# Kernel tuning notes

Measured on AMD Instinct MI355X. Metric: run time of the kernel, lower is better.

The kernel has to match this reference:

```python
import jax, jax.numpy as jnp
import numpy as np

B, T, D, P = 4, 2048, 1024, 128

def setup_inputs() -> dict:
    key = jax.random.key(0)
    ks = jax.random.split(key, 10)
    inp = {
        "x": jax.random.normal(ks[0], (B, T, D), dtype=jnp.float32),
        "Q_filt": jax.random.normal(ks[1], (P, P), dtype=jnp.float32),
        "K_filt": jax.random.normal(ks[2], (P, P), dtype=jnp.float32),
        "W_in": jax.random.normal(ks[3], (D, P), dtype=jnp.float32) / np.sqrt(D),
        "b_in": jax.random.normal(ks[4], (P,), dtype=jnp.float32) * 0.01,
        "W_v": jax.random.normal(ks[5], (D, P), dtype=jnp.float32) / np.sqrt(D),
        "b_v": jax.random.normal(ks[6], (P,), dtype=jnp.float32) * 0.01,
        "W_o": jax.random.normal(ks[7], (P, D), dtype=jnp.float32) / np.sqrt(P),
        "b_o": jax.random.normal(ks[8], (D,), dtype=jnp.float32) * 0.01,
        "decay": jnp.ones((T,), dtype=jnp.float32),
    }
    return inp

def reference(x, Q_filt, K_filt, W_in, b_in, W_v, b_v, W_o, b_o, decay):
    # x: (B,T,D)
    x_proj = x @ W_in + b_in          # (B,T,P)
    Q = x_proj @ Q_filt               # (B,T,P)
    K = x_proj @ K_filt               # (B,T,P)
    V = x @ W_v + b_v                 # (B,T,P)
    # outer-product state per timestep, scaled by per-step decay
    Z = jnp.einsum('bti,btj->btij', V, K) * decay[None, :, None, None]
    H = jnp.cumsum(Z, axis=1)         # (B,T,P,P) cumulative linear-attn state
    Y = jnp.einsum('bti,btij->btj', Q, H)  # (B,T,P)
    return Y @ W_o + b_o              # (B,T,D)
```

## Files before the change

kernel.cpp:

```cpp
#include <hip/hip_runtime.h>

#define BB 4
#define TT 2048
#define DD 1024
#define PP 128
#define NC 16
#define CH 128

typedef __attribute__((ext_vector_type(8))) short bf16x8;
typedef __attribute__((ext_vector_type(4))) float f32x4;

__device__ inline ushort f2bf(float f) {
  unsigned u = __builtin_bit_cast(unsigned, f);
  u = (u + 0x7FFF + ((u >> 16) & 1)) >> 16;
  return (ushort)u;
}

__device__ inline void gll16(const void* g, void* l) {
  __builtin_amdgcn_global_load_lds(
      (const __attribute__((address_space(1))) void*)g,
      (__attribute__((address_space(3))) void*)l, 16, 0, 0);
}

__device__ inline int swzoff(int row, int kbyte) {
  return row * 256 + (kbyte ^ ((row & 7) << 4));
}

template <int NI, int NT>
__device__ inline void stage_swz(const ushort* __restrict__ g, int ld, int koff,
                                 char* lds, int tid) {
#pragma unroll
  for (int j = 0; j < NI; ++j) {
    int L = j * (NT * 16) + tid * 16;
    int row = L >> 8;
    int off = (L & 255) ^ ((row & 7) << 4);
    gll16(g + (size_t)row * ld + koff + (off >> 1),
          lds + j * (NT * 16) + ((tid & (NT - 64)) << 4));
  }
}

__device__ inline bf16x8 ld_swz(const char* lds, int row, int kbyte) {
  return *(const bf16x8*)(lds + swzoff(row, kbyte));
}

__device__ inline bf16x8 pack8(const float4& a, const float4& b) {
  bf16x8 v;
  v[0] = (short)f2bf(a.x); v[1] = (short)f2bf(a.y);
  v[2] = (short)f2bf(a.z); v[3] = (short)f2bf(a.w);
  v[4] = (short)f2bf(b.x); v[5] = (short)f2bf(b.y);
  v[6] = (short)f2bf(b.z); v[7] = (short)f2bf(b.w);
  return v;
}

__global__ __launch_bounds__(256) void prep_w(
    const float* __restrict__ Qf, const float* __restrict__ Kf,
    const float* __restrict__ W_in, const float* __restrict__ b_in,
    const float* __restrict__ W_v, const float* __restrict__ b_v,
    const float* __restrict__ W_o, ushort* __restrict__ WcatT,
    ushort* __restrict__ QKcT, ushort* __restrict__ WoT,
    float* __restrict__ bcat) {
  int i = blockIdx.x * 256 + threadIdx.x;
  if (i < 262144) {
    int n = i & 255, k = i >> 8;
    float v = (n < 128) ? W_in[k * 128 + n] : W_v[k * 128 + (n - 128)];
    WcatT[(size_t)n * 1024 + k] = f2bf(v);
  } else if (i < 294912) {
    int j = i - 262144;
    int n = j & 255, k = j >> 8;
    float v = (n < 128) ? Qf[k * 128 + n] : Kf[k * 128 + (n - 128)];
    QKcT[n * 128 + k] = f2bf(v);
  } else if (i < 425984) {
    int j = i - 294912;
    int n = j & 1023, k = j >> 10;
    WoT[(size_t)n * 128 + k] = f2bf(W_o[(size_t)k * 1024 + n]);
  } else if (i < 426240) {
    int j = i - 425984;
    bcat[j] = (j < 128) ? b_in[j] : b_v[j - 128];
  }
}

__global__ __launch_bounds__(512) void gemm_xw(
    const float* __restrict__ x, const ushort* __restrict__ WcatT,
    const float* __restrict__ bcat, ushort* __restrict__ XP,
    ushort* __restrict__ V, ushort* __restrict__ VT) {
  __shared__ char sm[2][49152];
  const int bid = blockIdx.x;
  const int swz = (bid & 7) * 32 + (bid >> 3);
  const int bm = (swz >> 1) * 64;
  const int bn = (swz & 1) * 128;
  const int tid = threadIdx.x, w = tid >> 6, l = tid & 63;
  const int wr = w >> 2, wc = w & 3, lr = l & 15, lk = l >> 4;

  const int arow = tid >> 3;
  const int acol = (tid & 7) * 16;
  const float* Ax = x + (size_t)(bm + arow) * DD + acol;
  const ushort* Bg = WcatT + (size_t)bn * DD;

  float4 ra[4];
  f32x4 z = {0.f, 0.f, 0.f, 0.f};
  f32x4 acc[2][2];
#pragma unroll
  for (int m = 0; m < 2; ++m)
#pragma unroll
    for (int n = 0; n < 2; ++n) acc[m][n] = z;

#define LOADA(t)                                                  \
  {                                                               \
    const float4* p = (const float4*)(Ax + (((t) & 7) << 7));     \
    _Pragma("unroll") for (int j = 0; j < 4; ++j) ra[j] = p[j];   \
  }
#define WRITEA(lds)                                               \
  {                                                               \
    *(bf16x8*)((lds) + swzoff(arow, acol * 2)) = pack8(ra[0], ra[1]); \
    *(bf16x8*)((lds) + swzoff(arow, acol * 2 + 16)) = pack8(ra[2], ra[3]); \
  }

  LOADA(0);
  stage_swz<4, 512>(Bg, DD, 0, sm[0] + 16384, tid);
  asm volatile("s_waitcnt vmcnt(4)" ::: "memory");
  WRITEA(sm[0]);
  LOADA(1);

  int cur = 0;
  for (int t = 0; t < 8; ++t) {
    char* nxt = sm[cur ^ 1];
    stage_swz<4, 512>(Bg, DD, ((t + 1) & 7) << 7, nxt + 16384, tid);
    asm volatile("s_waitcnt vmcnt(4)" ::: "memory");
    WRITEA(nxt);
    LOADA(t + 2);
    asm volatile("s_waitcnt lgkmcnt(0)" ::: "memory");
    __builtin_amdgcn_s_barrier();
    const char* cp = sm[cur];
#pragma unroll
    for (int ks = 0; ks < 4; ++ks) {
      const int kb = ks * 64 + lk * 16;
      bf16x8 af[2], bfp[2];
#pragma unroll
      for (int m = 0; m < 2; ++m) af[m] = ld_swz(cp, wr * 32 + m * 16 + lr, kb);
#pragma unroll
      for (int n = 0; n < 2; ++n)
        bfp[n] = ld_swz(cp + 16384, wc * 32 + n * 16 + lr, kb);
#pragma unroll
      for (int m = 0; m < 2; ++m)
#pragma unroll
        for (int n = 0; n < 2; ++n)
          acc[m][n] = __builtin_amdgcn_mfma_f32_16x16x32_bf16(af[m], bfp[n], acc[m][n], 0, 0, 0);
    }
    __builtin_amdgcn_s_barrier();
    cur ^= 1;
  }
  asm volatile("s_waitcnt vmcnt(0)" ::: "memory");
#undef LOADA
#undef WRITEA

#pragma unroll
  for (int m = 0; m < 2; ++m)
#pragma unroll
    for (int n = 0; n < 2; ++n) {
      const int rowb = bm + wr * 32 + m * 16 + lk * 4;
      const int col = bn + wc * 32 + n * 16 + lr;
      const float bv = bcat[col];
      if (bn == 0) {
#pragma unroll
        for (int j = 0; j < 4; ++j)
          XP[(size_t)(rowb + j) * PP + col] = f2bf(acc[m][n][j] + bv);
      } else {
        const int cc = col - 128;
        ushort4 pk;
#pragma unroll
        for (int j = 0; j < 4; ++j) {
          ushort u = f2bf(acc[m][n][j] + bv);
          V[(size_t)(rowb + j) * PP + cc] = u;
          ((ushort*)&pk)[j] = u;
        }
        *(ushort4*)&VT[(size_t)cc * (BB * TT) + rowb] = pk;
      }
    }
}

__global__ __launch_bounds__(512) void qk_state(
    const ushort* __restrict__ XP, const ushort* __restrict__ QKcT,
    const ushort* __restrict__ VT, const float* __restrict__ decay,
    ushort* __restrict__ Qb, ushort* __restrict__ KT,
    float* __restrict__ Sc) {
  __shared__ char sm[98304];
  char* smA = sm;
  char* smB = sm + 32768;
  const int bc = blockIdx.x;
  const size_t r0 = (size_t)(bc >> 4) * TT + (bc & 15) * CH;
  const int tid = threadIdx.x, w = tid >> 6, l = tid & 63;
  const int wr = w >> 2, wc = w & 3, lr = l & 15, lk = l >> 4;

  stage_swz<4, 512>(XP + r0 * PP, PP, 0, smA, tid);
  stage_swz<8, 512>(QKcT, PP, 0, smB, tid);

  f32x4 z = {0.f, 0.f, 0.f, 0.f};
  f32x4 acc[4][4];
#pragma unroll
  for (int m = 0; m < 4; ++m)
#pragma unroll
    for (int n = 0; n < 4; ++n) acc[m][n] = z;
  __syncthreads();

#pragma unroll
  for (int ks = 0; ks < 4; ++ks) {
    const int kb = ks * 64 + lk * 16;
    bf16x8 af[4], bfp[4];
#pragma unroll
    for (int m = 0; m < 4; ++m) af[m] = ld_swz(smA, wr * 64 + m * 16 + lr, kb);
#pragma unroll
    for (int n = 0; n < 4; ++n)
      bfp[n] = ld_swz(smB, wc * 64 + n * 16 + lr, kb);
#pragma unroll
    for (int m = 0; m < 4; ++m)
#pragma unroll
      for (int n = 0; n < 4; ++n)
        acc[m][n] = __builtin_amdgcn_mfma_f32_16x16x32_bf16(af[m], bfp[n], acc[m][n], 0, 0, 0);
  }
  __syncthreads();

#pragma unroll
  for (int m = 0; m < 4; ++m)
#pragma unroll
    for (int n = 0; n < 4; ++n) {
      const int rowb = wr * 64 + m * 16 + lk * 4;
      const int col = wc * 64 + n * 16 + lr;
      if (col < 128) {
#pragma unroll
        for (int j = 0; j < 4; ++j)
          Qb[(r0 + rowb + j) * PP + col] = f2bf(acc[m][n][j]);
      } else {
        const int cc = col - 128;
        ushort4 pk;
#pragma unroll
        for (int j = 0; j < 4; ++j) {
          float v = acc[m][n][j];
          ((ushort*)&pk)[j] = f2bf(v);
          ushort kd = f2bf(v * decay[(r0 + rowb + j) & (TT - 1)]);
          *(ushort*)(smA + swzoff(cc, (rowb + j) * 2)) = kd;
        }
        *(ushort4*)&KT[(size_t)cc * (BB * TT) + r0 + rowb] = pk;
      }
    }
  __syncthreads();

  f32x4 a2[4][2];
#pragma unroll
  for (int m = 0; m < 4; ++m)
#pragma unroll
    for (int n = 0; n < 2; ++n) a2[m][n] = z;
#pragma unroll
  for (int ks = 0; ks < 4; ++ks) {
    const int kb = ks * 64 + lk * 16, kk = ks * 32 + lk * 8;
    bf16x8 af[4], bfp[2];
#pragma unroll
    for (int m = 0; m < 4; ++m) af[m] = ld_swz(smA, wr * 64 + m * 16 + lr, kb);
#pragma unroll
    for (int n = 0; n < 2; ++n)
      bfp[n] = *(const bf16x8*)&VT[(size_t)(wc * 32 + n * 16 + lr) * (BB * TT) + r0 + kk];
#pragma unroll
    for (int m = 0; m < 4; ++m)
#pragma unroll
      for (int n = 0; n < 2; ++n)
        a2[m][n] = __builtin_amdgcn_mfma_f32_16x16x32_bf16(af[m], bfp[n], a2[m][n], 0, 0, 0);
  }
#pragma unroll
  for (int m = 0; m < 4; ++m)
#pragma unroll
    for (int n = 0; n < 2; ++n)
#pragma unroll
      for (int j = 0; j < 4; ++j)
        Sc[(size_t)bc * 16384 + (size_t)(wr * 64 + m * 16 + lk * 4 + j) * 128 +
           (wc * 32 + n * 16 + lr)] = a2[m][n][j];
}

__global__ __launch_bounds__(256) void chunk_scan(const float* __restrict__ Sc,
                                                  ushort* __restrict__ SxT) {
  int b = blockIdx.y;
  int e = blockIdx.x * 256 + threadIdx.x;
  float run = 0.f;
#pragma unroll
  for (int c = 0; c < NC; ++c) {
    size_t idx = ((size_t)(b * NC + c)) * 16384 + e;
    SxT[idx] = f2bf(run);
    run += Sc[idx];
  }
}

__global__ __launch_bounds__(256) void attn_mfma(
    const ushort* __restrict__ Qb, const ushort* __restrict__ V,
    const ushort* __restrict__ KT, const ushort* __restrict__ SxT,
    const float* __restrict__ decay, ushort* __restrict__ Y) {
  __shared__ char Am[64 * 256];
  const int blk = blockIdx.x;
  const int bc = blk >> 2, hr = (blk >> 1) & 1, hc = blk & 1;
  const int b = bc >> 4, c = bc & 15;
  const size_t r0 = (size_t)b * TT + c * CH;
  const int tid = threadIdx.x, w = tid >> 6, l = tid & 63;
  const int wr = w >> 1, wc = w & 1, lr = l & 15, lk = l >> 4;
  const float* dc = decay + c * CH;

  f32x4 z = {0.f, 0.f, 0.f, 0.f};
  f32x4 a1[2][4];
#pragma unroll
  for (int m = 0; m < 2; ++m)
#pragma unroll
    for (int n = 0; n < 4; ++n) a1[m][n] = z;

#pragma unroll
  for (int ks = 0; ks < 4; ++ks) {
    const int kk = ks * 32 + lk * 8;
    bf16x8 af[2], bf[4];
#pragma unroll
    for (int m = 0; m < 2; ++m)
      af[m] = *(const bf16x8*)&Qb[(r0 + hr * 64 + wr * 32 + m * 16 + lr) * 128 + kk];
#pragma unroll
    for (int n = 0; n < 4; ++n)
      bf[n] = *(const bf16x8*)&V[(r0 + wc * 64 + n * 16 + lr) * 128 + kk];
#pragma unroll
    for (int m = 0; m < 2; ++m)
#pragma unroll
      for (int n = 0; n < 4; ++n)
        a1[m][n] = __builtin_amdgcn_mfma_f32_16x16x32_bf16(af[m], bf[n], a1[m][n], 0, 0, 0);
  }
#pragma unroll
  for (int m = 0; m < 2; ++m)
#pragma unroll
    for (int n = 0; n < 4; ++n)
#pragma unroll
      for (int j = 0; j < 4; ++j) {
        int tl = wr * 32 + m * 16 + lk * 4 + j;
        int t = hr * 64 + tl;
        int s = wc * 64 + n * 16 + lr;
        float v = (s <= t) ? a1[m][n][j] * dc[s] : 0.f;
        *(ushort*)(Am + swzoff(tl, s * 2)) = f2bf(v);
      }
  __syncthreads();

  f32x4 a2[2][2];
#pragma unroll
  for (int m = 0; m < 2; ++m)
#pragma unroll
    for (int n = 0; n < 2; ++n) a2[m][n] = z;
#pragma unroll
  for (int ks = 0; ks < 4; ++ks) {
    const int kb = ks * 64 + lk * 16, kk = ks * 32 + lk * 8;
    bf16x8 af[2], bf[2];
#pragma unroll
    for (int m = 0; m < 2; ++m)
      af[m] = ld_swz(Am, wr * 32 + m * 16 + lr, kb);
#pragma unroll
    for (int n = 0; n < 2; ++n)
      bf[n] = *(const bf16x8*)&KT[(size_t)(hc * 64 + wc * 32 + n * 16 + lr) * (BB * TT) + r0 + kk];
#pragma unroll
    for (int m = 0; m < 2; ++m)
#pragma unroll
      for (int n = 0; n < 2; ++n)
        a2[m][n] = __builtin_amdgcn_mfma_f32_16x16x32_bf16(af[m], bf[n], a2[m][n], 0, 0, 0);
  }
#pragma unroll
  for (int ks = 0; ks < 4; ++ks) {
    const int kk = ks * 32 + lk * 8;
    bf16x8 af[2], bf[2];
#pragma unroll
    for (int m = 0; m < 2; ++m)
      af[m] = *(const bf16x8*)&Qb[(r0 + hr * 64 + wr * 32 + m * 16 + lr) * 128 + kk];
#pragma unroll
    for (int n = 0; n < 2; ++n)
      bf[n] = *(const bf16x8*)&SxT[(size_t)bc * 16384 +
                                   (size_t)(hc * 64 + wc * 32 + n * 16 + lr) * 128 + kk];
#pragma unroll
    for (int m = 0; m < 2; ++m)
#pragma unroll
      for (int n = 0; n < 2; ++n)
        a2[m][n] = __builtin_amdgcn_mfma_f32_16x16x32_bf16(af[m], bf[n], a2[m][n], 0, 0, 0);
  }
#pragma unroll
  for (int m = 0; m < 2; ++m)
#pragma unroll
    for (int n = 0; n < 2; ++n)
#pragma unroll
      for (int j = 0; j < 4; ++j) {
        int t = hr * 64 + wr * 32 + m * 16 + lk * 4 + j;
        int col = hc * 64 + wc * 32 + n * 16 + lr;
        Y[(r0 + t) * 128 + col] = f2bf(a2[m][n][j]);
      }
}

__global__ __launch_bounds__(256) void gemm_out(
    const ushort* __restrict__ Y, const ushort* __restrict__ WoT,
    const float* __restrict__ b_o, float* __restrict__ out) {
  __shared__ char sm[49152];
  const int bid = blockIdx.x;
  const int swz = (bid & 7) * 128 + (bid >> 3);
  const int bm = (swz >> 3) * 64, bn = (swz & 7) * 128;
  const int tid = threadIdx.x, w = tid >> 6, l = tid & 63;
  const int wr = w >> 1, wc = w & 1, lr = l & 15, lk = l >> 4;
  stage_swz<4, 256>(Y + (size_t)bm * PP, PP, 0, sm, tid);
  stage_swz<8, 256>(WoT + (size_t)bn * PP, PP, 0, sm + 16384, tid);
  f32x4 z = {0.f, 0.f, 0.f, 0.f};
  f32x4 acc[2][4];
#pragma unroll
  for (int m = 0; m < 2; ++m)
#pragma unroll
    for (int n = 0; n < 4; ++n) acc[m][n] = z;
  __syncthreads();
#pragma unroll
  for (int ks = 0; ks < 4; ++ks) {
    const int kb = ks * 64 + lk * 16;
    bf16x8 af[2], bfp[4];
#pragma unroll
    for (int m = 0; m < 2; ++m) af[m] = ld_swz(sm, wr * 32 + m * 16 + lr, kb);
#pragma unroll
    for (int n = 0; n < 4; ++n)
      bfp[n] = ld_swz(sm + 16384, wc * 64 + n * 16 + lr, kb);
#pragma unroll
    for (int m = 0; m < 2; ++m)
#pragma unroll
      for (int n = 0; n < 4; ++n)
        acc[m][n] = __builtin_amdgcn_mfma_f32_16x16x32_bf16(af[m], bfp[n], acc[m][n], 0, 0, 0);
  }
#pragma unroll
  for (int m = 0; m < 2; ++m)
#pragma unroll
    for (int n = 0; n < 4; ++n) {
      const int rowb = bm + wr * 32 + m * 16 + lk * 4;
      const int col = bn + wc * 64 + n * 16 + lr;
      const float bv = b_o[col];
#pragma unroll
      for (int j = 0; j < 4; ++j)
        out[(size_t)(rowb + j) * DD + col] = acc[m][n][j] + bv;
    }
}

extern "C" void kernel_launch(void* const* d_in, const int* in_sizes, int n_in,
                              void* d_out, int out_size, void* d_ws, size_t ws_size,
                              hipStream_t stream) {
  const float* x = (const float*)d_in[0];
  const float* Qf = (const float*)d_in[1];
  const float* Kf = (const float*)d_in[2];
  const float* W_in = (const float*)d_in[3];
  const float* b_in = (const float*)d_in[4];
  const float* W_v = (const float*)d_in[5];
  const float* b_v = (const float*)d_in[6];
  const float* W_o = (const float*)d_in[7];
  const float* b_o = (const float*)d_in[8];
  const float* decay = (const float*)d_in[9];
  float* out = (float*)d_out;
  char* W = (char*)d_ws;

  ushort* XP    = (ushort*)(W);
  ushort* V     = (ushort*)(W + 2097152);
  ushort* VT    = (ushort*)(W + 4194304);
  ushort* Qb    = (ushort*)(W + 6291456);
  ushort* KT    = (ushort*)(W + 8388608);
  float*  Sc    = (float*)(W + 10485760);
  ushort* SxT   = (ushort*)(W + 14680064);
  ushort* Yb    = (ushort*)(W + 16777216);
  ushort* WcatT = (ushort*)(W + 18874368);
  ushort* QKcT  = (ushort*)(W + 19398656);
  ushort* WoT   = (ushort*)(W + 19464192);
  float*  bcat  = (float*)(W + 19726336);

  prep_w<<<1665, 256, 0, stream>>>(Qf, Kf, W_in, b_in, W_v, b_v, W_o,
                                   WcatT, QKcT, WoT, bcat);
  gemm_xw<<<256, 512, 0, stream>>>(x, WcatT, bcat, XP, V, VT);
  qk_state<<<BB * NC, 512, 0, stream>>>(XP, QKcT, VT, decay, Qb, KT, Sc);
  chunk_scan<<<dim3(64, BB), 256, 0, stream>>>(Sc, SxT);
  attn_mfma<<<4 * BB * NC, 256, 0, stream>>>(Qb, V, KT, SxT, decay, Yb);
  gemm_out<<<1024, 256, 0, stream>>>(Yb, WoT, b_o, out);
}
```

Baseline: 56.35 us.

## Tile weight transposes, shrink GEMM K-tile, split chunk-state blocks, store decayed K

The weight prep kernel now transposes 64x64 tiles through LDS, giving coalesced reads and writes in place of a scattered per-element transpose. The input GEMM halves its K-tile to 64, cutting LDS per block so more blocks can reside, and writes VT through an LDS transpose to get wide stores. qk_state is split into two half-chunk blocks per chunk to double the grid, and chunk_scan sums the two partial states. K is stored already multiplied by decay, which removes the decay multiply from attn_mfma. The cost is more loop iterations in the GEMM, extra partial-state memory traffic, and a larger workspace.

```diff
diff --git a/kernel.cpp b/kernel.cpp
--- a/kernel.cpp
+++ b/kernel.cpp
@@ -25,6 +25,9 @@
 __device__ inline int swzoff(int row, int kbyte) {
   return row * 256 + (kbyte ^ ((row & 7) << 4));
 }
+__device__ inline int swz128(int row, int kbyte) {
+  return row * 128 + (kbyte ^ ((row & 7) << 4));
+}
 
 template <int NI, int NT>
 __device__ inline void stage_swz(const ushort* __restrict__ g, int ld, int koff,
@@ -38,9 +41,24 @@
           lds + j * (NT * 16) + ((tid & (NT - 64)) << 4));
   }
 }
+template <int NI, int NT>
+__device__ inline void stage_swz128(const ushort* __restrict__ g, int ld,
+                                    int koff, char* lds, int tid) {
+#pragma unroll
+  for (int j = 0; j < NI; ++j) {
+    int L = j * (NT * 16) + tid * 16;
+    int row = L >> 7;
+    int off = (L & 127) ^ ((row & 7) << 4);
+    gll16(g + (size_t)row * ld + koff + (off >> 1),
+          lds + j * (NT * 16) + ((tid & (NT - 64)) << 4));
+  }
+}
 
 __device__ inline bf16x8 ld_swz(const char* lds, int row, int kbyte) {
   return *(const bf16x8*)(lds + swzoff(row, kbyte));
+}
+__device__ inline bf16x8 ld_swz128(const char* lds, int row, int kbyte) {
+  return *(const bf16x8*)(lds + swz128(row, kbyte));
 }
 
 __device__ inline bf16x8 pack8(const float4& a, const float4& b) {
@@ -52,38 +70,75 @@
   return v;
 }
 
-__global__ __launch_bounds__(256) void prep_w(
+__global__ __launch_bounds__(256) void prep_t(
     const float* __restrict__ Qf, const float* __restrict__ Kf,
     const float* __restrict__ W_in, const float* __restrict__ b_in,
     const float* __restrict__ W_v, const float* __restrict__ b_v,
     const float* __restrict__ W_o, ushort* __restrict__ WcatT,
     ushort* __restrict__ QKcT, ushort* __restrict__ WoT,
     float* __restrict__ bcat) {
-  int i = blockIdx.x * 256 + threadIdx.x;
-  if (i < 262144) {
-    int n = i & 255, k = i >> 8;
-    float v = (n < 128) ? W_in[k * 128 + n] : W_v[k * 128 + (n - 128)];
-    WcatT[(size_t)n * 1024 + k] = f2bf(v);
-  } else if (i < 294912) {
-    int j = i - 262144;
-    int n = j & 255, k = j >> 8;
-    float v = (n < 128) ? Qf[k * 128 + n] : Kf[k * 128 + (n - 128)];
-    QKcT[n * 128 + k] = f2bf(v);
-  } else if (i < 425984) {
-    int j = i - 294912;
-    int n = j & 1023, k = j >> 10;
-    WoT[(size_t)n * 128 + k] = f2bf(W_o[(size_t)k * 1024 + n]);
-  } else if (i < 426240) {
-    int j = i - 425984;
-    bcat[j] = (j < 128) ? b_in[j] : b_v[j - 128];
-  }
-}
-
-__global__ __launch_bounds__(512) void gemm_xw(
+  const int bid = blockIdx.x;
+  const int t = threadIdx.x;
+  if (bid == 104) {
+    bcat[t] = (t < 128) ? b_in[t] : b_v[t - 128];
+    return;
+  }
+  const float* src;
+  ushort* dst;
+  int ld_src, ld_dst, nn0;
+  if (bid < 64) {
+    int tn = bid >> 4, tk = bid & 15;
+    src = (tn < 2) ? W_in : W_v;
+    nn0 = (tn & 1) * 64;
+    ld_src = 128;
+    src += (size_t)(tk * 64) * 128;
+    dst = WcatT + (size_t)(tn * 64) * 1024 + tk * 64;
+    ld_dst = 1024;
+  } else if (bid < 96) {
+    int j = bid - 64, tn = j >> 1, tk = j & 1;
+    src = W_o;
+    nn0 = tn * 64;
+    ld_src = 1024;
+    src += (size_t)(tk * 64) * 1024;
+    dst = WoT + (size_t)(tn * 64) * 128 + tk * 64;
+    ld_dst = 128;
+  } else {
+    int j = bid - 96, tn = j >> 1, tk = j & 1;
+    src = (tn < 2) ? Qf : Kf;
+    nn0 = (tn & 1) * 64;
+    ld_src = 128;
+    src += (size_t)(tk * 64) * 128;
+    dst = QKcT + (size_t)(tn * 64) * 128 + tk * 64;
+    ld_dst = 128;
+  }
+  __shared__ ushort Tt[64][68];
+  const int kr = t >> 4, nc = (t & 15) * 4;
+#pragma unroll
+  for (int p = 0; p < 4; ++p) {
+    float4 v = *(const float4*)&src[(size_t)(p * 16 + kr) * ld_src + nn0 + nc];
+    Tt[p * 16 + kr][nc + 0] = f2bf(v.x);
+    Tt[p * 16 + kr][nc + 1] = f2bf(v.y);
+    Tt[p * 16 + kr][nc + 2] = f2bf(v.z);
+    Tt[p * 16 + kr][nc + 3] = f2bf(v.w);
+  }
+  __syncthreads();
+  const int nr = t >> 4, kc = (t & 15) * 4;
+#pragma unroll
+  for (int p = 0; p < 4; ++p) {
+    ushort4 o;
+    o.x = Tt[kc + 0][p * 16 + nr];
+    o.y = Tt[kc + 1][p * 16 + nr];
+    o.z = Tt[kc + 2][p * 16 + nr];
+    o.w = Tt[kc + 3][p * 16 + nr];
+    *(ushort4*)&dst[(size_t)(p * 16 + nr) * ld_dst + kc] = o;
+  }
+}
+
+__global__ __launch_bounds__(512, 4) void gemm_xw(
     const float* __restrict__ x, const ushort* __restrict__ WcatT,
     const float* __restrict__ bcat, ushort* __restrict__ XP,
     ushort* __restrict__ V, ushort* __restrict__ VT) {
-  __shared__ char sm[2][49152];
+  __shared__ char sm[2][24576];
   const int bid = blockIdx.x;
   const int swz = (bid & 7) * 32 + (bid >> 3);
   const int bm = (swz >> 1) * 64;
@@ -92,11 +147,11 @@
   const int wr = w >> 2, wc = w & 3, lr = l & 15, lk = l >> 4;
 
   const int arow = tid >> 3;
-  const int acol = (tid & 7) * 16;
+  const int acol = (tid & 7) * 8;
   const float* Ax = x + (size_t)(bm + arow) * DD + acol;
   const ushort* Bg = WcatT + (size_t)bn * DD;
 
-  float4 ra[4];
+  float4 ra[2];
   f32x4 z = {0.f, 0.f, 0.f, 0.f};
   f32x4 acc[2][2];
 #pragma unroll
@@ -104,42 +159,41 @@
 #pragma unroll
     for (int n = 0; n < 2; ++n) acc[m][n] = z;
 
-#define LOADA(t)                                                  \
-  {                                                               \
-    const float4* p = (const float4*)(Ax + (((t) & 7) << 7));     \
-    _Pragma("unroll") for (int j = 0; j < 4; ++j) ra[j] = p[j];   \
-  }
-#define WRITEA(lds)                                               \
-  {                                                               \
-    *(bf16x8*)((lds) + swzoff(arow, acol * 2)) = pack8(ra[0], ra[1]); \
-    *(bf16x8*)((lds) + swzoff(arow, acol * 2 + 16)) = pack8(ra[2], ra[3]); \
-  }
+#define LOADA(t)                                                 \
+  {                                                              \
+    const float4* p = (const float4*)(Ax + (((t) & 15) << 6));   \
+    ra[0] = p[0];                                                \
+    ra[1] = p[1];                                                \
+  }
+#define WRITEA(lds) \
+  { *(bf16x8*)((lds) + swz128(arow, acol * 2)) = pack8(ra[0], ra[1]); }
 
   LOADA(0);
-  stage_swz<4, 512>(Bg, DD, 0, sm[0] + 16384, tid);
-  asm volatile("s_waitcnt vmcnt(4)" ::: "memory");
+  stage_swz128<2, 512>(Bg, DD, 0, sm[0] + 8192, tid);
+  asm volatile("s_waitcnt vmcnt(2)" ::: "memory");
   WRITEA(sm[0]);
   LOADA(1);
 
   int cur = 0;
-  for (int t = 0; t < 8; ++t) {
+  for (int t = 0; t < 16; ++t) {
     char* nxt = sm[cur ^ 1];
-    stage_swz<4, 512>(Bg, DD, ((t + 1) & 7) << 7, nxt + 16384, tid);
-    asm volatile("s_waitcnt vmcnt(4)" ::: "memory");
+    stage_swz128<2, 512>(Bg, DD, ((t + 1) & 15) << 6, nxt + 8192, tid);
+    asm volatile("s_waitcnt vmcnt(2)" ::: "memory");
     WRITEA(nxt);
     LOADA(t + 2);
     asm volatile("s_waitcnt lgkmcnt(0)" ::: "memory");
     __builtin_amdgcn_s_barrier();
     const char* cp = sm[cur];
 #pragma unroll
-    for (int ks = 0; ks < 4; ++ks) {
+    for (int ks = 0; ks < 2; ++ks) {
       const int kb = ks * 64 + lk * 16;
       bf16x8 af[2], bfp[2];
 #pragma unroll
-      for (int m = 0; m < 2; ++m) af[m] = ld_swz(cp, wr * 32 + m * 16 + lr, kb);
+      for (int m = 0; m < 2; ++m)
+        af[m] = ld_swz128(cp, wr * 32 + m * 16 + lr, kb);
 #pragma unroll
       for (int n = 0; n < 2; ++n)
-        bfp[n] = ld_swz(cp + 16384, wc * 32 + n * 16 + lr, kb);
+        bfp[n] = ld_swz128(cp + 8192, wc * 32 + n * 16 + lr, kb);
 #pragma unroll
       for (int m = 0; m < 2; ++m)
 #pragma unroll
@@ -153,111 +207,135 @@
 #undef LOADA
 #undef WRITEA
 
-#pragma unroll
-  for (int m = 0; m < 2; ++m)
-#pragma unroll
-    for (int n = 0; n < 2; ++n) {
-      const int rowb = bm + wr * 32 + m * 16 + lk * 4;
-      const int col = bn + wc * 32 + n * 16 + lr;
-      const float bv = bcat[col];
-      if (bn == 0) {
+  if (bn == 0) {
+#pragma unroll
+    for (int m = 0; m < 2; ++m)
+#pragma unroll
+      for (int n = 0; n < 2; ++n) {
+        const int rowb = bm + wr * 32 + m * 16 + lk * 4;
+        const int col = wc * 32 + n * 16 + lr;
+        const float bv = bcat[col];
 #pragma unroll
         for (int j = 0; j < 4; ++j)
           XP[(size_t)(rowb + j) * PP + col] = f2bf(acc[m][n][j] + bv);
+      }
+  } else {
+    ushort(*VTt)[72] = (ushort(*)[72]) & sm[0][0];
+#pragma unroll
+    for (int m = 0; m < 2; ++m)
+#pragma unroll
+      for (int n = 0; n < 2; ++n) {
+        const int tl = wr * 32 + m * 16 + lk * 4;
+        const int cc = wc * 32 + n * 16 + lr;
+        const float bv = bcat[128 + cc];
+#pragma unroll
+        for (int j = 0; j < 4; ++j) {
+          ushort u = f2bf(acc[m][n][j] + bv);
+          V[(size_t)(bm + tl + j) * PP + cc] = u;
+          VTt[cc][tl + j] = u;
+        }
+      }
+    __syncthreads();
+    const int row = tid >> 2;
+#pragma unroll
+    for (int i = 0; i < 2; ++i) {
+      const int ch = (tid & 3) * 2 + i;
+      bf16x8 v = *(const bf16x8*)&VTt[row][ch * 8];
+      *(bf16x8*)&VT[(size_t)row * (BB * TT) + bm + ch * 8] = v;
+    }
+  }
+}
+
+__global__ __launch_bounds__(512, 4) void qk_state(
+    const ushort* __restrict__ XP, const ushort* __restrict__ QKcT,
+    const ushort* __restrict__ VT, const float* __restrict__ decay,
+    ushort* __restrict__ Qb, ushort* __restrict__ KdT,
+    float* __restrict__ Sc2) {
+  __shared__ char sm[81920];
+  char* smA = sm;
+  char* smB = sm + 16384;
+  const int blk = blockIdx.x;
+  const int bc = blk >> 1, mh = blk & 1;
+  const size_t r0 = (size_t)(bc >> 4) * TT + (bc & 15) * CH;
+  const size_t rh = r0 + mh * 64;
+  const int tid = threadIdx.x, w = tid >> 6, l = tid & 63;
+  const int wr = w >> 2, wc = w & 3, lr = l & 15, lk = l >> 4;
+
+  stage_swz<2, 512>(XP + rh * PP, PP, 0, smA, tid);
+  stage_swz<8, 512>(QKcT, PP, 0, smB, tid);
+
+  f32x4 z = {0.f, 0.f, 0.f, 0.f};
+  f32x4 acc[2][4];
+#pragma unroll
+  for (int m = 0; m < 2; ++m)
+#pragma unroll
+    for (int n = 0; n < 4; ++n) acc[m][n] = z;
+  __syncthreads();
+
+#pragma unroll
+  for (int ks = 0; ks < 4; ++ks) {
+    const int kb = ks * 64 + lk * 16;
+    bf16x8 af[2], bfp[4];
+#pragma unroll
+    for (int m = 0; m < 2; ++m) af[m] = ld_swz(smA, wr * 32 + m * 16 + lr, kb);
+#pragma unroll
+    for (int n = 0; n < 4; ++n)
+      bfp[n] = ld_swz(smB, wc * 64 + n * 16 + lr, kb);
+#pragma unroll
+    for (int m = 0; m < 2; ++m)
+#pragma unroll
+      for (int n = 0; n < 4; ++n)
+        acc[m][n] = __builtin_amdgcn_mfma_f32_16x16x32_bf16(af[m], bfp[n], acc[m][n], 0, 0, 0);
+  }
+  __syncthreads();
+
+#pragma unroll
+  for (int m = 0; m < 2; ++m)
+#pragma unroll
+    for (int n = 0; n < 4; ++n) {
+      const int rowl = wr * 32 + m * 16 + lk * 4;
+      const int col = wc * 64 + n * 16 + lr;
+      if (col < 128) {
+#pragma unroll
+        for (int j = 0; j < 4; ++j)
+          Qb[(rh + rowl + j) * PP + col] = f2bf(acc[m][n][j]);
       } else {
         const int cc = col - 128;
-        ushort4 pk;
 #pragma unroll
         for (int j = 0; j < 4; ++j) {
-          ushort u = f2bf(acc[m][n][j] + bv);
-          V[(size_t)(rowb + j) * PP + cc] = u;
-          ((ushort*)&pk)[j] = u;
+          float v = acc[m][n][j] * decay[(rh + rowl + j) & (TT - 1)];
+          *(ushort*)(smA + swz128(cc, (rowl + j) * 2)) = f2bf(v);
         }
-        *(ushort4*)&VT[(size_t)cc * (BB * TT) + rowb] = pk;
-      }
-    }
-}
-
-__global__ __launch_bounds__(512) void qk_state(
-    const ushort* __restrict__ XP, const ushort* __restrict__ QKcT,
-    const ushort* __restrict__ VT, const float* __restrict__ decay,
-    ushort* __restrict__ Qb, ushort* __restrict__ KT,
-    float* __restrict__ Sc) {
-  __shared__ char sm[98304];
-  char* smA = sm;
-  char* smB = sm + 32768;
-  const int bc = blockIdx.x;
-  const size_t r0 = (size_t)(bc >> 4) * TT + (bc & 15) * CH;
-  const int tid = threadIdx.x, w = tid >> 6, l = tid & 63;
-  const int wr = w >> 2, wc = w & 3, lr = l & 15, lk = l >> 4;
-
-  stage_swz<4, 512>(XP + r0 * PP, PP, 0, smA, tid);
-  stage_swz<8, 512>(QKcT, PP, 0, smB, tid);
-
-  f32x4 z = {0.f, 0.f, 0.f, 0.f};
-  f32x4 acc[4][4];
-#pragma unroll
-  for (int m = 0; m < 4; ++m)
-#pragma unroll
-    for (int n = 0; n < 4; ++n) acc[m][n] = z;
-  __syncthreads();
-
-#pragma unroll
-  for (int ks = 0; ks < 4; ++ks) {
-    const int kb = ks * 64 + lk * 16;
-    bf16x8 af[4], bfp[4];
-#pragma unroll
-    for (int m = 0; m < 4; ++m) af[m] = ld_swz(smA, wr * 64 + m * 16 + lr, kb);
-#pragma unroll
-    for (int n = 0; n < 4; ++n)
-      bfp[n] = ld_swz(smB, wc * 64 + n * 16 + lr, kb);
-#pragma unroll
-    for (int m = 0; m < 4; ++m)
-#pragma unroll
-      for (int n = 0; n < 4; ++n)
-        acc[m][n] = __builtin_amdgcn_mfma_f32_16x16x32_bf16(af[m], bfp[n], acc[m][n], 0, 0, 0);
-  }
-  __syncthreads();
-
-#pragma unroll
-  for (int m = 0; m < 4; ++m)
-#pragma unroll
-    for (int n = 0; n < 4; ++n) {
-      const int rowb = wr * 64 + m * 16 + lk * 4;
-      const int col = wc * 64 + n * 16 + lr;
-      if (col < 128) {
-#pragma unroll
-        for (int j = 0; j < 4; ++j)
-          Qb[(r0 + rowb + j) * PP + col] = f2bf(acc[m][n][j]);
-      } else {
-        const int cc = col - 128;
-        ushort4 pk;
-#pragma unroll
-        for (int j = 0; j < 4; ++j) {
-          float v = acc[m][n][j];
-          ((ushort*)&pk)[j] = f2bf(v);
-          ushort kd = f2bf(v * decay[(r0 + rowb + j) & (TT - 1)]);
-          *(ushort*)(smA + swzoff(cc, (rowb + j) * 2)) = kd;
-        }
-        *(ushort4*)&KT[(size_t)cc * (BB * TT) + r0 + rowb] = pk;
       }
     }
   __syncthreads();
 
+  {
+    const int cc = tid >> 2;
+#pragma unroll
+    for (int i = 0; i < 2; ++i) {
+      const int ch = (tid & 3) * 2 + i;
+      bf16x8 v = ld_swz128(smA, cc, ch * 16);
+      *(bf16x8*)&KdT[(size_t)cc * (BB * TT) + rh + ch * 8] = v;
+    }
+  }
+
   f32x4 a2[4][2];
 #pragma unroll
   for (int m = 0; m < 4; ++m)
 #pragma unroll
     for (int n = 0; n < 2; ++n) a2[m][n] = z;
 #pragma unroll
-  for (int ks = 0; ks < 4; ++ks) {
-    const int kb = ks * 64 + lk * 16, kk = ks * 32 + lk * 8;
+  for (int ks = 0; ks < 2; ++ks) {
+    const int kb = ks * 64 + lk * 16;
+    const int kk = ks * 32 + lk * 8;
     bf16x8 af[4], bfp[2];
 #pragma unroll
-    for (int m = 0; m < 4; ++m) af[m] = ld_swz(smA, wr * 64 + m * 16 + lr, kb);
+    for (int m = 0; m < 4; ++m)
+      af[m] = ld_swz128(smA, wr * 64 + m * 16 + lr, kb);
 #pragma unroll
     for (int n = 0; n < 2; ++n)
-      bfp[n] = *(const bf16x8*)&VT[(size_t)(wc * 32 + n * 16 + lr) * (BB * TT) + r0 + kk];
+      bfp[n] = *(const bf16x8*)&VT[(size_t)(wc * 32 + n * 16 + lr) * (BB * TT) + rh + kk];
 #pragma unroll
     for (int m = 0; m < 4; ++m)
 #pragma unroll
@@ -270,27 +348,28 @@
     for (int n = 0; n < 2; ++n)
 #pragma unroll
       for (int j = 0; j < 4; ++j)
-        Sc[(size_t)bc * 16384 + (size_t)(wr * 64 + m * 16 + lk * 4 + j) * 128 +
-           (wc * 32 + n * 16 + lr)] = a2[m][n][j];
-}
-
-__global__ __launch_bounds__(256) void chunk_scan(const float* __restrict__ Sc,
+        Sc2[((size_t)bc * 2 + mh) * 16384 +
+            (size_t)(wr * 64 + m * 16 + lk * 4 + j) * 128 +
+            (wc * 32 + n * 16 + lr)] = a2[m][n][j];
+}
+
+__global__ __launch_bounds__(256) void chunk_scan(const float* __restrict__ Sc2,
                                                   ushort* __restrict__ SxT) {
-  int b = blockIdx.y;
-  int e = blockIdx.x * 256 + threadIdx.x;
+  const int b = blockIdx.y;
+  const int e = blockIdx.x * 256 + threadIdx.x;
   float run = 0.f;
 #pragma unroll
   for (int c = 0; c < NC; ++c) {
-    size_t idx = ((size_t)(b * NC + c)) * 16384 + e;
-    SxT[idx] = f2bf(run);
-    run += Sc[idx];
+    const size_t bc = (size_t)(b * NC + c);
+    SxT[bc * 16384 + e] = f2bf(run);
+    run += Sc2[bc * 2 * 16384 + e] + Sc2[(bc * 2 + 1) * 16384 + e];
   }
 }
 
 __global__ __launch_bounds__(256) void attn_mfma(
     const ushort* __restrict__ Qb, const ushort* __restrict__ V,
-    const ushort* __restrict__ KT, const ushort* __restrict__ SxT,
-    const float* __restrict__ decay, ushort* __restrict__ Y) {
+    const ushort* __restrict__ KdT, const ushort* __restrict__ SxT,
+    ushort* __restrict__ Y) {
   __shared__ char Am[64 * 256];
   const int blk = blockIdx.x;
   const int bc = blk >> 2, hr = (blk >> 1) & 1, hc = blk & 1;
@@ -298,7 +377,6 @@
   const size_t r0 = (size_t)b * TT + c * CH;
   const int tid = threadIdx.x, w = tid >> 6, l = tid & 63;
   const int wr = w >> 1, wc = w & 1, lr = l & 15, lk = l >> 4;
-  const float* dc = decay + c * CH;
 
   f32x4 z = {0.f, 0.f, 0.f, 0.f};
   f32x4 a1[2][4];
@@ -332,7 +410,7 @@
         int tl = wr * 32 + m * 16 + lk * 4 + j;
         int t = hr * 64 + tl;
         int s = wc * 64 + n * 16 + lr;
-        float v = (s <= t) ? a1[m][n][j] * dc[s] : 0.f;
+        float v = (s <= t) ? a1[m][n][j] : 0.f;
         *(ushort*)(Am + swzoff(tl, s * 2)) = f2bf(v);
       }
   __syncthreads();
@@ -351,7 +429,7 @@
       af[m] = ld_swz(Am, wr * 32 + m * 16 + lr, kb);
 #pragma unroll
     for (int n = 0; n < 2; ++n)
-      bf[n] = *(const bf16x8*)&KT[(size_t)(hc * 64 + wc * 32 + n * 16 + lr) * (BB * TT) + r0 + kk];
+      bf[n] = *(const bf16x8*)&KdT[(size_t)(hc * 64 + wc * 32 + n * 16 + lr) * (BB * TT) + r0 + kk];
 #pragma unroll
     for (int m = 0; m < 2; ++m)
 #pragma unroll
@@ -453,20 +531,20 @@
   ushort* V     = (ushort*)(W + 2097152);
   ushort* VT    = (ushort*)(W + 4194304);
   ushort* Qb    = (ushort*)(W + 6291456);
-  ushort* KT    = (ushort*)(W + 8388608);
-  float*  Sc    = (float*)(W + 10485760);
-  ushort* SxT   = (ushort*)(W + 14680064);
-  ushort* Yb    = (ushort*)(W + 16777216);
-  ushort* WcatT = (ushort*)(W + 18874368);
-  ushort* QKcT  = (ushort*)(W + 19398656);
-  ushort* WoT   = (ushort*)(W + 19464192);
-  float*  bcat  = (float*)(W + 19726336);
-
-  prep_w<<<1665, 256, 0, stream>>>(Qf, Kf, W_in, b_in, W_v, b_v, W_o,
-                                   WcatT, QKcT, WoT, bcat);
+  ushort* KdT   = (ushort*)(W + 8388608);
+  float*  Sc2   = (float*)(W + 10485760);
+  ushort* SxT   = (ushort*)(W + 18874368);
+  ushort* Yb    = (ushort*)(W + 20971520);
+  ushort* WcatT = (ushort*)(W + 23068672);
+  ushort* QKcT  = (ushort*)(W + 23592960);
+  ushort* WoT   = (ushort*)(W + 23658496);
+  float*  bcat  = (float*)(W + 23920640);
+
+  prep_t<<<105, 256, 0, stream>>>(Qf, Kf, W_in, b_in, W_v, b_v, W_o,
+                                  WcatT, QKcT, WoT, bcat);
   gemm_xw<<<256, 512, 0, stream>>>(x, WcatT, bcat, XP, V, VT);
-  qk_state<<<BB * NC, 512, 0, stream>>>(XP, QKcT, VT, decay, Qb, KT, Sc);
-  chunk_scan<<<dim3(64, BB), 256, 0, stream>>>(Sc, SxT);
-  attn_mfma<<<4 * BB * NC, 256, 0, stream>>>(Qb, V, KT, SxT, decay, Yb);
+  qk_state<<<2 * BB * NC, 512, 0, stream>>>(XP, QKcT, VT, decay, Qb, KdT, Sc2);
+  chunk_scan<<<dim3(64, BB), 256, 0, stream>>>(Sc2, SxT);
+  attn_mfma<<<4 * BB * NC, 256, 0, stream>>>(Qb, V, KdT, SxT, Yb);
   gemm_out<<<1024, 256, 0, stream>>>(Yb, WoT, b_o, out);
 }
```

Measured after the change: 50.99 us. 1.11x faster.
